# Kernel optimization log

Hardware: AMD Instinct MI355X
Metric: run time of the kernel (lower is better)

## Reference

```python
import jax, jax.numpy as jnp
import numpy as np

N_E = 1024
E_DIM = 256
BETA = 0.25

def setup_inputs() -> dict:
    key = jax.random.key(0)
    k1, k2 = jax.random.split(key)
    z = jax.random.normal(k1, (32, E_DIM, 32, 32), dtype=jnp.float32)
    # embedding initialized uniform(-1/n_e, 1/n_e) as in the torch module
    emb_w = jax.random.uniform(k2, (N_E, E_DIM), dtype=jnp.float32,
                               minval=-1.0 / N_E, maxval=1.0 / N_E)
    return {"z": z, "emb_w": emb_w}

def reference(z, emb_w):
    # z: (B, C, H, W) with C == e_dim
    zp = jnp.transpose(z, (0, 2, 3, 1))          # (B, H, W, C)
    zf = zp.reshape(-1, emb_w.shape[1])           # (N, e_dim)
    # squared L2 distances: ||z||^2 + ||e||^2 - 2 z e^T  -> (N, n_e)
    d = (jnp.sum(zf * zf, axis=1, keepdims=True)
         + jnp.sum(emb_w * emb_w, axis=1)
         - 2.0 * jnp.matmul(zf, emb_w.T))
    idx = jnp.argmin(d, axis=1)                   # (N,)
    min_encoding_indices = idx[:, None]           # (N, 1)
    min_encodings = jax.nn.one_hot(idx, emb_w.shape[0], dtype=zf.dtype)  # (N, n_e)
    z_q = emb_w[idx].reshape(zp.shape)            # gather instead of one-hot matmul
    # VQ loss (stop-gradient on codebook / encoder respectively)
    loss = (jnp.mean((jax.lax.stop_gradient(z_q) - zp) ** 2)
            + BETA * jnp.mean((z_q - jax.lax.stop_gradient(zp)) ** 2))
    # straight-through estimator
    z_q_st = zp + jax.lax.stop_gradient(z_q - zp)
    e_mean = jnp.mean(min_encodings, axis=0)      # (n_e,)
    perplexity = jnp.exp(-jnp.sum(e_mean * jnp.log(e_mean + 1e-10)))
    z_q_out = jnp.transpose(z_q_st, (0, 3, 1, 2)) # (B, C, H, W)
    return (z_q_out, loss, perplexity, min_encodings, min_encoding_indices)
```

## Files before the change

kernel.cpp:

```cpp
#include <hip/hip_runtime.h>
#include <math.h>

#define NROWS 32768
#define NE    1024
#define CDIM  256
#define ZB_STRIDE 262144

#define ZQ_OFF   0
#define LOSS_OFF 8388608
#define PERP_OFF 8388609
#define ENC_OFF  8388610
#define IDX_OFF  41943042

#define THETA 1.0e-4f
#define NEG2_SCALE (-0.00048828125f)

typedef _Float16 f16x8 __attribute__((ext_vector_type(8)));
typedef __attribute__((ext_vector_type(4))) float f32x4;
typedef __attribute__((ext_vector_type(8))) unsigned short ushort8;

__device__ __forceinline__ unsigned short f2h(float x) {
  _Float16 h = (_Float16)x;
  unsigned short u;
  __builtin_memcpy(&u, &h, 2);
  return u;
}

__device__ __forceinline__ float np_sumsq_256_s1(const float* __restrict__ base) {
  float tot[2];
#pragma unroll
  for (int hh = 0; hh < 2; ++hh) {
    float r[8];
#pragma unroll
    for (int j = 0; j < 8; ++j) {
      float x = base[hh * 128 + j];
      r[j] = __fmul_rn(x, x);
    }
    for (int i = 8; i < 128; i += 8) {
#pragma unroll
      for (int j = 0; j < 8; ++j) {
        float x = base[hh * 128 + i + j];
        r[j] = __fadd_rn(r[j], __fmul_rn(x, x));
      }
    }
    tot[hh] = __fadd_rn(__fadd_rn(__fadd_rn(r[0], r[1]), __fadd_rn(r[2], r[3])),
                        __fadd_rn(__fadd_rn(r[4], r[5]), __fadd_rn(r[6], r[7])));
  }
  return __fadd_rn(tot[0], tot[1]);
}

__global__ __launch_bounds__(256) void convert_all(const float* __restrict__ z,
                                                   const float* __restrict__ emb,
                                                   unsigned short* __restrict__ zf16r,
                                                   unsigned short* __restrict__ ef16r,
                                                   float* __restrict__ embT,
                                                   float* __restrict__ znorm,
                                                   float* __restrict__ enorm) {
  __shared__ __align__(16) char smem[38144];
  const int bid = blockIdx.x;
  const int t = threadIdx.x;

  if (bid < 512) {
    unsigned short (*T16)[266] = reinterpret_cast<unsigned short (*)[266]>(smem);
    float (*accsF)[8][16][4] = reinterpret_cast<float (*)[8][16][4]>(smem + 34048);
    const int b = bid >> 4, hwt = bid & 15;
    const int hw0 = hwt * 64;
    const int hw4 = t & 15;
    const int jj = (t >> 4) & 7;
    const int hh = t >> 7;
    const float* zb = z + (size_t)b * ZB_STRIDE + hw0 + hw4 * 4;

    float rr[4];
#pragma unroll
    for (int i = 0; i < 16; ++i) {
      int c = hh * 128 + jj + 8 * i;
      float4 v = *reinterpret_cast<const float4*>(zb + (size_t)c * 1024);
      const float xv[4] = {v.x, v.y, v.z, v.w};
#pragma unroll
      for (int q = 0; q < 4; ++q) {
        float p = __fmul_rn(xv[q], xv[q]);
        rr[q] = (i == 0) ? p : __fadd_rn(rr[q], p);
        T16[hw4 * 4 + q][c] = f2h(xv[q]);
      }
    }
#pragma unroll
    for (int q = 0; q < 4; ++q) accsF[hh][jj][hw4][q] = rr[q];
    __syncthreads();

    if (t < 64) {
      const int h4 = t >> 2, cq = t & 3;
      float tot[2];
#pragma unroll
      for (int half = 0; half < 2; ++half) {
        float r[8];
#pragma unroll
        for (int j = 0; j < 8; ++j) r[j] = accsF[half][j][h4][cq];
        tot[half] = __fadd_rn(__fadd_rn(__fadd_rn(r[0], r[1]), __fadd_rn(r[2], r[3])),
                              __fadd_rn(__fadd_rn(r[4], r[5]), __fadd_rn(r[6], r[7])));
      }
      znorm[b * 1024 + hw0 + t] = __fadd_rn(tot[0], tot[1]);
    }

    const int pw = b * 16 + hwt;
    const int panel = pw >> 1, wrh = pw & 1;
    const int l15w = t & 15, gw = (t >> 4) & 3, miw = t >> 6;
    const int rowW = miw * 16 + l15w;
#pragma unroll
    for (int kc = 0; kc < 8; ++kc) {
      ushort8 o;
#pragma unroll
      for (int el = 0; el < 8; ++el) o[el] = T16[rowW][kc * 32 + gw * 8 + el];
      size_t chunk = ((((size_t)panel * 2 + wrh) * 8 + kc) * 4 + miw) * 64 + (size_t)gw * 16 + l15w;
      *reinterpret_cast<ushort8*>(zf16r + (chunk << 3)) = o;
    }
  } else if (bid < 640) {
    int cid = (bid - 512) * 256 + t;
    int e = cid >> 5, cc = cid & 31;
    int kc = cc >> 2, g = cc & 3;
    int c0 = kc * 32 + g * 8;
    ushort8 o;
#pragma unroll
    for (int el = 0; el < 8; ++el) o[el] = f2h(emb[(size_t)e * 256 + c0 + el] * 4096.0f);
    int et = e >> 7, wcb = (e >> 6) & 1, nj = (e >> 4) & 3, l15e = e & 15;
    size_t chunk = ((((size_t)et * 2 + wcb) * 8 + kc) * 4 + nj) * 64 + (size_t)g * 16 + l15e;
    *reinterpret_cast<ushort8*>(ef16r + (chunk << 3)) = o;
  } else if (bid < 896) {
    float (*tile)[33] = reinterpret_cast<float (*)[33]>(smem);
    int tb = bid - 640;
    int be = tb & 31, bc = tb >> 5;
    int tx = t & 31, ty = t >> 5;
#pragma unroll
    for (int i = 0; i < 4; ++i)
      tile[ty + 8 * i][tx] = emb[(size_t)(be * 32 + ty + 8 * i) * 256 + bc * 32 + tx];
    __syncthreads();
#pragma unroll
    for (int i = 0; i < 4; ++i)
      embT[(size_t)(bc * 32 + ty + 8 * i) * 1024 + be * 32 + tx] = tile[tx][ty + 8 * i];
  } else {
    int n = (bid - 896) * 256 + t;
    enorm[n] = np_sumsq_256_s1(emb + (size_t)n * CDIM);
  }
}

__global__ __launch_bounds__(256, 4) void argmin_tile(
    const unsigned short* __restrict__ zf16r, const unsigned short* __restrict__ ef16r,
    const float* __restrict__ znorm, const float* __restrict__ enorm,
    float* __restrict__ pbd, int* __restrict__ pbi, float* __restrict__ pb2) {
  __shared__ float sdd[128][2];
  __shared__ float sd2[128][2];
  __shared__ int   sdi[128][2];

  const int tid = threadIdx.x;
  const int lane = tid & 63, w = tid >> 6;
  const int wr = w >> 1, wc = w & 1;
  const int l15 = lane & 15, g = lane >> 4;

  const int bid = blockIdx.x;
  const int nb2 = (bid >> 3) & 1;
  const int mb = (bid & 7) * 32 + (bid >> 4);
  const int n0 = mb * 128;

  const unsigned short* bP0 = zf16r + (size_t)(mb * 2 + wc) * 16384 + lane * 8;

  const int n0w = n0 + wc * 64;
  float zn[4];
#pragma unroll
  for (int nj = 0; nj < 4; ++nj) zn[nj] = znorm[n0w + nj * 16 + l15];

  float bd[4], b2[4]; int bi[4];
#pragma unroll
  for (int nj = 0; nj < 4; ++nj) { bd[nj] = 3.4e38f; b2[nj] = 3.4e38f; bi[nj] = 0; }

  const f32x4 z4 = {0.f, 0.f, 0.f, 0.f};
#pragma unroll 1
  for (int et = 0; et < 4; ++et) {
    const unsigned short* aP = ef16r + (size_t)(nb2 * 8 + et * 2 + wr) * 16384 + lane * 8;
    const unsigned short* bP = bP0;

    f32x4 acc[4][4];
#pragma unroll
    for (int ei = 0; ei < 4; ++ei)
#pragma unroll
      for (int nj = 0; nj < 4; ++nj) acc[ei][nj] = z4;

#pragma unroll 1
    for (int kc = 0; kc < 8; ++kc) {
      f16x8 af[4], bv[4];
#pragma unroll
      for (int ei = 0; ei < 4; ++ei)
        af[ei] = *reinterpret_cast<const f16x8*>(aP + ei * 512);
#pragma unroll
      for (int nj = 0; nj < 4; ++nj)
        bv[nj] = *reinterpret_cast<const f16x8*>(bP + nj * 512);
      aP += 2048; bP += 2048;
#pragma unroll
      for (int ei = 0; ei < 4; ++ei)
#pragma unroll
        for (int nj = 0; nj < 4; ++nj)
          acc[ei][nj] = __builtin_amdgcn_mfma_f32_16x16x32_f16(af[ei], bv[nj],
                                                               acc[ei][nj], 0, 0, 0);
    }

    const int e0w = nb2 * 512 + et * 128 + wr * 64;
#pragma unroll
    for (int ei = 0; ei < 4; ++ei)
#pragma unroll
      for (int rg = 0; rg < 4; ++rg) {
        int e = e0w + ei * 16 + g * 4 + rg;
        float en = enorm[e];
#pragma unroll
        for (int nj = 0; nj < 4; ++nj) {
          float d = fmaf(NEG2_SCALE, acc[ei][nj][rg], __fadd_rn(zn[nj], en));
          if (d < bd[nj]) {
            b2[nj] = bd[nj]; bd[nj] = d; bi[nj] = e;
          } else if (d < b2[nj]) {
            b2[nj] = d;
          }
        }
      }
  }

#pragma unroll
  for (int nj = 0; nj < 4; ++nj) {
#pragma unroll
    for (int m = 16; m <= 32; m <<= 1) {
      float od = __shfl_xor(bd[nj], m, 64);
      int   oi = __shfl_xor(bi[nj], m, 64);
      float o2 = __shfl_xor(b2[nj], m, 64);
      float hi = fmaxf(bd[nj], od);
      b2[nj] = fminf(fminf(b2[nj], o2), hi);
      if (od < bd[nj] || (od == bd[nj] && oi < bi[nj])) { bd[nj] = od; bi[nj] = oi; }
    }
    if (g == 0) {
      int nl = wc * 64 + nj * 16 + l15;
      sdd[nl][wr] = bd[nj];
      sdi[nl][wr] = bi[nj];
      sd2[nl][wr] = b2[nj];
    }
  }
  __syncthreads();

  if (tid < 128) {
    float d0 = sdd[tid][0], d1 = sdd[tid][1];
    int   i0 = sdi[tid][0], i1 = sdi[tid][1];
    float s0 = sd2[tid][0], s1 = sd2[tid][1];
    float bdf; int bif;
    if (d1 < d0 || (d1 == d0 && i1 < i0)) { bdf = d1; bif = i1; } else { bdf = d0; bif = i0; }
    float b2f = fminf(fminf(s0, s1), fmaxf(d0, d1));
    size_t o = (size_t)(n0 + tid) * 2 + nb2;
    pbd[o] = bdf; pbi[o] = bif; pb2[o] = b2f;
  }
}

__global__ __launch_bounds__(256) void merge_kernel(
    const float* __restrict__ pbd, const int* __restrict__ pbi,
    const float* __restrict__ pb2,
    int* __restrict__ idx_out, float* __restrict__ loss_blk,
    int* __restrict__ flag_cnt, int* __restrict__ flag_list) {
  __shared__ float red[256];
  const int t = threadIdx.x;
  int n = blockIdx.x * 256 + t;
  float d0 = pbd[(size_t)n * 2], d1 = pbd[(size_t)n * 2 + 1];
  int   i0 = pbi[(size_t)n * 2], i1 = pbi[(size_t)n * 2 + 1];
  float s0 = pb2[(size_t)n * 2], s1 = pb2[(size_t)n * 2 + 1];
  float bd; int bi;
  if (d1 < d0 || (d1 == d0 && i1 < i0)) { bd = d1; bi = i1; } else { bd = d0; bi = i0; }
  float b2 = fminf(fminf(s0, s1), fmaxf(d0, d1));
  idx_out[n] = bi;
  if (b2 - bd < THETA) {
    int p = atomicAdd(flag_cnt, 1);
    flag_list[p] = n;
  }
  red[t] = bd;
  __syncthreads();
  for (int s2 = 128; s2 > 0; s2 >>= 1) {
    if (t < s2) red[t] += red[t + s2];
    __syncthreads();
  }
  if (t == 0) loss_blk[blockIdx.x] = red[0];
}

__global__ __launch_bounds__(256) void repair_kernel(
    const float* __restrict__ z, const float* __restrict__ embT,
    const float* __restrict__ znorm, const float* __restrict__ enorm,
    const int* __restrict__ flag_cnt, const int* __restrict__ flag_list,
    int* __restrict__ idx_out) {
  __shared__ float zrow[4][256];
  __shared__ float rd[256];
  __shared__ int   ri[256];
  const int t = threadIdx.x;
  const int cnt = flag_cnt[0] < NROWS ? flag_cnt[0] : NROWS;
  const int nquad = (cnt + 3) >> 2;
  const float4* embT4 = reinterpret_cast<const float4*>(embT);
  for (int j = blockIdx.x; j < nquad; j += gridDim.x) {
    int nr[4];
    __syncthreads();
#pragma unroll
    for (int r = 0; r < 4; ++r) {
      int jr = j * 4 + r;
      nr[r] = flag_list[jr < cnt ? jr : cnt - 1];
      zrow[r][t] = z[(size_t)(nr[r] >> 10) * ZB_STRIDE + (size_t)t * 1024 + (nr[r] & 1023)];
    }
    __syncthreads();
    float4 dot[4] = {{0.f,0.f,0.f,0.f},{0.f,0.f,0.f,0.f},{0.f,0.f,0.f,0.f},{0.f,0.f,0.f,0.f}};
    for (int k = 0; k < 256; ++k) {
      float4 v = embT4[k * 256 + t];
#pragma unroll
      for (int r = 0; r < 4; ++r) {
        float s = zrow[r][k];
        dot[r].x = fmaf(s, v.x, dot[r].x);
        dot[r].y = fmaf(s, v.y, dot[r].y);
        dot[r].z = fmaf(s, v.z, dot[r].z);
        dot[r].w = fmaf(s, v.w, dot[r].w);
      }
    }
#pragma unroll 1
    for (int r = 0; r < 4; ++r) {
      const float zn = znorm[nr[r]];
      float bd = 3.4e38f; int bi = 0;
      const float dv[4] = {dot[r].x, dot[r].y, dot[r].z, dot[r].w};
#pragma unroll
      for (int q = 0; q < 4; ++q) {
        int e = t * 4 + q;
        float d = __fsub_rn(__fadd_rn(zn, enorm[e]), __fmul_rn(2.0f, dv[q]));
        if (d < bd) { bd = d; bi = e; }
      }
      rd[t] = bd; ri[t] = bi;
      __syncthreads();
      for (int s2 = 128; s2 > 0; s2 >>= 1) {
        if (t < s2) {
          float od = rd[t + s2]; int oi = ri[t + s2];
          if (od < rd[t] || (od == rd[t] && oi < ri[t])) { rd[t] = od; ri[t] = oi; }
        }
        __syncthreads();
      }
      if (t == 0) idx_out[nr[r]] = ri[0];
      __syncthreads();
    }
  }
}

__global__ __launch_bounds__(256) void outputs_kernel(const int* __restrict__ idx,
                                                      const float* __restrict__ emb,
                                                      float* __restrict__ out_enc,
                                                      float* __restrict__ out_idxf,
                                                      int* __restrict__ hist,
                                                      float* __restrict__ zq_out) {
  const int t = threadIdx.x;
  for (int i = blockIdx.x * 256 + t; i < NROWS * 256; i += 2048 * 256) {
    int n = i >> 8, j4 = i & 255;
    int e = idx[n];
    float4 v = {0.f, 0.f, 0.f, 0.f};
    if ((e >> 2) == j4) ((float*)&v)[e & 3] = 1.0f;
    reinterpret_cast<float4*>(out_enc)[i] = v;
  }
  if (blockIdx.x < 1024) {
    __shared__ int   sidx[32];
    __shared__ float erow[32][257];
    int b = blockIdx.x >> 5, h = blockIdx.x & 31;
    if (t < 32) sidx[t] = idx[b * 1024 + h * 32 + t];
    __syncthreads();
    const float4* emb4 = reinterpret_cast<const float4*>(emb);
    int rj = t >> 3, v0 = t & 7;
    int er = sidx[rj];
#pragma unroll
    for (int u = 0; u < 8; ++u) {
      int f4 = v0 + 8 * u;
      float4 vv = emb4[(size_t)er * 64 + f4];
      erow[rj][f4 * 4 + 0] = vv.x;
      erow[rj][f4 * 4 + 1] = vv.y;
      erow[rj][f4 * 4 + 2] = vv.z;
      erow[rj][f4 * 4 + 3] = vv.w;
    }
    __syncthreads();
    int w4 = t & 7, cs = t >> 3;
    float4* zq4 = reinterpret_cast<float4*>(zq_out + (size_t)b * ZB_STRIDE + h * 32);
#pragma unroll
    for (int u = 0; u < 8; ++u) {
      int c = cs + 32 * u;
      float4 o = {erow[w4 * 4 + 0][c], erow[w4 * 4 + 1][c],
                  erow[w4 * 4 + 2][c], erow[w4 * 4 + 3][c]};
      zq4[(size_t)c * 256 + w4] = o;
    }
  } else if (blockIdx.x < 1152) {
    int n = (blockIdx.x - 1024) * 256 + t;
    int e = idx[n];
    out_idxf[n] = (float)e;
    atomicAdd(&hist[e], 1);
  }
}

__global__ __launch_bounds__(256) void finalize_kernel(const float* __restrict__ loss_blk,
                                                       const int* __restrict__ hist,
                                                       float* __restrict__ out_loss,
                                                       float* __restrict__ out_perp) {
  __shared__ float red[256];
  int t = threadIdx.x;
  red[t] = (t < 128) ? loss_blk[t] : 0.f;
  __syncthreads();
  for (int s2 = 128; s2 > 0; s2 >>= 1) {
    if (t < s2) red[t] += red[t + s2];
    __syncthreads();
  }
  if (t == 0) out_loss[0] = 1.25f * (red[0] / 8388608.0f);
  __syncthreads();
  float hs = 0.f;
  for (int i = t; i < 1024; i += 256) {
    float em = (float)hist[i] / 32768.0f;
    hs += em * logf(em + 1e-10f);
  }
  red[t] = hs;
  __syncthreads();
  for (int s2 = 128; s2 > 0; s2 >>= 1) {
    if (t < s2) red[t] += red[t + s2];
    __syncthreads();
  }
  if (t == 0) out_perp[0] = expf(-red[0]);
}

extern "C" void kernel_launch(void* const* d_in, const int* in_sizes, int n_in,
                              void* d_out, int out_size, void* d_ws, size_t ws_size,
                              hipStream_t stream) {
  const float* z   = (const float*)d_in[0];
  const float* emb = (const float*)d_in[1];
  float* out = (float*)d_out;

  float* out_zq   = out + ZQ_OFF;
  float* out_loss = out + LOSS_OFF;
  float* out_perp = out + PERP_OFF;
  float* out_enc  = out + ENC_OFF;
  float* out_idxf = out + IDX_OFF;

  int*   idx       = (int*)d_ws;
  int*   hist      = idx + NROWS;
  int*   flag_cnt  = hist + NE;
  int*   flag_list = flag_cnt + 4;
  float* loss_blk  = (float*)(flag_list + NROWS);
  float* znorm     = loss_blk + 128;
  float* enorm     = znorm + NROWS;

  unsigned short* zf16r = (unsigned short*)(out_enc + 2);
  unsigned short* ef16r = zf16r + (size_t)NROWS * CDIM;
  float*          embT  = (float*)(ef16r + (size_t)NE * CDIM);
  float*          pbd   = embT + 262144;
  int*            pbi   = (int*)(pbd + 65536);
  float*          pb2   = (float*)(pbi + 65536);

  hipMemsetAsync(hist, 0, (NE + 1) * sizeof(int), stream);

  convert_all<<<900, 256, 0, stream>>>(z, emb, zf16r, ef16r, embT, znorm, enorm);
  argmin_tile<<<512, 256, 0, stream>>>(zf16r, ef16r, znorm, enorm, pbd, pbi, pb2);
  merge_kernel<<<NROWS / 256, 256, 0, stream>>>(pbd, pbi, pb2, idx, loss_blk, flag_cnt, flag_list);
  repair_kernel<<<256, 256, 0, stream>>>(z, embT, znorm, enorm, flag_cnt, flag_list, idx);
  outputs_kernel<<<2048, 256, 0, stream>>>(idx, emb, out_enc, out_idxf, hist, out_zq);
  finalize_kernel<<<1, 256, 0, stream>>>(loss_blk, hist, out_loss, out_perp);
}
```

Before: 157.4 us.

## Give each argmin block all codes for 64 rows and drop merge kernel

The argmin kernel now assigns each block 64 rows across all 1024 codes, with the four waves each covering 256 codes, instead of 128 rows across half the codebook. The cross-half merge therefore happens inside the block, and the block writes final indices, flags near-ties and sums loss partials directly. This removes the separate merge kernel launch and the global partial-result buffers. In exchange, each block reuses its z tile over more codes but gets less reuse of the embedding tile, and the loss partials grow to 512 entries, which the finalize kernel now reduces.

```diff
diff --git a/kernel.cpp b/kernel.cpp
--- a/kernel.cpp
+++ b/kernel.cpp
@@ -145,27 +145,25 @@
 __global__ __launch_bounds__(256, 4) void argmin_tile(
     const unsigned short* __restrict__ zf16r, const unsigned short* __restrict__ ef16r,
     const float* __restrict__ znorm, const float* __restrict__ enorm,
-    float* __restrict__ pbd, int* __restrict__ pbi, float* __restrict__ pb2) {
-  __shared__ float sdd[128][2];
-  __shared__ float sd2[128][2];
-  __shared__ int   sdi[128][2];
+    int* __restrict__ idx_out, float* __restrict__ loss_blk,
+    int* __restrict__ flag_cnt, int* __restrict__ flag_list) {
+  __shared__ float sdd[64][4];
+  __shared__ float sd2[64][4];
+  __shared__ int   sdi[64][4];
 
   const int tid = threadIdx.x;
   const int lane = tid & 63, w = tid >> 6;
-  const int wr = w >> 1, wc = w & 1;
   const int l15 = lane & 15, g = lane >> 4;
 
   const int bid = blockIdx.x;
-  const int nb2 = (bid >> 3) & 1;
-  const int mb = (bid & 7) * 32 + (bid >> 4);
-  const int n0 = mb * 128;
-
-  const unsigned short* bP0 = zf16r + (size_t)(mb * 2 + wc) * 16384 + lane * 8;
-
-  const int n0w = n0 + wc * 64;
+  const int mb = (bid & 7) * 64 + (bid >> 3);
+  const int n0 = mb * 64;
+
+  const unsigned short* bP0 = zf16r + (size_t)mb * 16384 + lane * 8;
+
   float zn[4];
 #pragma unroll
-  for (int nj = 0; nj < 4; ++nj) zn[nj] = znorm[n0w + nj * 16 + l15];
+  for (int nj = 0; nj < 4; ++nj) zn[nj] = znorm[n0 + nj * 16 + l15];
 
   float bd[4], b2[4]; int bi[4];
 #pragma unroll
@@ -174,7 +172,7 @@
   const f32x4 z4 = {0.f, 0.f, 0.f, 0.f};
 #pragma unroll 1
   for (int et = 0; et < 4; ++et) {
-    const unsigned short* aP = ef16r + (size_t)(nb2 * 8 + et * 2 + wr) * 16384 + lane * 8;
+    const unsigned short* aP = ef16r + (size_t)(w * 4 + et) * 16384 + lane * 8;
     const unsigned short* bP = bP0;
 
     f32x4 acc[4][4];
@@ -201,7 +199,7 @@
                                                                acc[ei][nj], 0, 0, 0);
     }
 
-    const int e0w = nb2 * 512 + et * 128 + wr * 64;
+    const int e0w = (w * 4 + et) * 64;
 #pragma unroll
     for (int ei = 0; ei < 4; ++ei)
 #pragma unroll
@@ -232,52 +230,39 @@
       if (od < bd[nj] || (od == bd[nj] && oi < bi[nj])) { bd[nj] = od; bi[nj] = oi; }
     }
     if (g == 0) {
-      int nl = wc * 64 + nj * 16 + l15;
-      sdd[nl][wr] = bd[nj];
-      sdi[nl][wr] = bi[nj];
-      sd2[nl][wr] = b2[nj];
+      int nl = nj * 16 + l15;
+      sdd[nl][w] = bd[nj];
+      sdi[nl][w] = bi[nj];
+      sd2[nl][w] = b2[nj];
     }
   }
   __syncthreads();
 
-  if (tid < 128) {
-    float d0 = sdd[tid][0], d1 = sdd[tid][1];
-    int   i0 = sdi[tid][0], i1 = sdi[tid][1];
-    float s0 = sd2[tid][0], s1 = sd2[tid][1];
-    float bdf; int bif;
-    if (d1 < d0 || (d1 == d0 && i1 < i0)) { bdf = d1; bif = i1; } else { bdf = d0; bif = i0; }
-    float b2f = fminf(fminf(s0, s1), fmaxf(d0, d1));
-    size_t o = (size_t)(n0 + tid) * 2 + nb2;
-    pbd[o] = bdf; pbi[o] = bif; pb2[o] = b2f;
-  }
-}
-
-__global__ __launch_bounds__(256) void merge_kernel(
-    const float* __restrict__ pbd, const int* __restrict__ pbi,
-    const float* __restrict__ pb2,
-    int* __restrict__ idx_out, float* __restrict__ loss_blk,
-    int* __restrict__ flag_cnt, int* __restrict__ flag_list) {
-  __shared__ float red[256];
-  const int t = threadIdx.x;
-  int n = blockIdx.x * 256 + t;
-  float d0 = pbd[(size_t)n * 2], d1 = pbd[(size_t)n * 2 + 1];
-  int   i0 = pbi[(size_t)n * 2], i1 = pbi[(size_t)n * 2 + 1];
-  float s0 = pb2[(size_t)n * 2], s1 = pb2[(size_t)n * 2 + 1];
-  float bd; int bi;
-  if (d1 < d0 || (d1 == d0 && i1 < i0)) { bd = d1; bi = i1; } else { bd = d0; bi = i0; }
-  float b2 = fminf(fminf(s0, s1), fmaxf(d0, d1));
-  idx_out[n] = bi;
-  if (b2 - bd < THETA) {
-    int p = atomicAdd(flag_cnt, 1);
-    flag_list[p] = n;
-  }
-  red[t] = bd;
-  __syncthreads();
-  for (int s2 = 128; s2 > 0; s2 >>= 1) {
-    if (t < s2) red[t] += red[t + s2];
-    __syncthreads();
-  }
-  if (t == 0) loss_blk[blockIdx.x] = red[0];
+  if (tid < 64) {
+    float bdf = 3.4e38f; int bif = 0x7FFFFFFF; int bw = -1;
+#pragma unroll
+    for (int ww = 0; ww < 4; ++ww) {
+      float d = sdd[tid][ww];
+      int   i = sdi[tid][ww];
+      if (d < bdf || (d == bdf && i < bif)) { bdf = d; bif = i; bw = ww; }
+    }
+    float b2f = 3.4e38f;
+#pragma unroll
+    for (int ww = 0; ww < 4; ++ww) {
+      float v = (ww == bw) ? sd2[tid][ww] : sdd[tid][ww];
+      b2f = fminf(b2f, v);
+    }
+    int n = n0 + tid;
+    idx_out[n] = bif;
+    if (b2f - bdf < THETA) {
+      int p = atomicAdd(flag_cnt, 1);
+      flag_list[p] = n;
+    }
+    float s = bdf;
+#pragma unroll
+    for (int m = 1; m <= 32; m <<= 1) s += __shfl_xor(s, m, 64);
+    if (tid == 0) loss_blk[bid] = s;
+  }
 }
 
 __global__ __launch_bounds__(256) void repair_kernel(
@@ -396,7 +381,7 @@
                                                        float* __restrict__ out_perp) {
   __shared__ float red[256];
   int t = threadIdx.x;
-  red[t] = (t < 128) ? loss_blk[t] : 0.f;
+  red[t] = loss_blk[t] + loss_blk[t + 256];
   __syncthreads();
   for (int s2 = 128; s2 > 0; s2 >>= 1) {
     if (t < s2) red[t] += red[t + s2];
@@ -436,21 +421,18 @@
   int*   flag_cnt  = hist + NE;
   int*   flag_list = flag_cnt + 4;
   float* loss_blk  = (float*)(flag_list + NROWS);
-  float* znorm     = loss_blk + 128;
+  float* znorm     = loss_blk + 512;
   float* enorm     = znorm + NROWS;
 
   unsigned short* zf16r = (unsigned short*)(out_enc + 2);
   unsigned short* ef16r = zf16r + (size_t)NROWS * CDIM;
   float*          embT  = (float*)(ef16r + (size_t)NE * CDIM);
-  float*          pbd   = embT + 262144;
-  int*            pbi   = (int*)(pbd + 65536);
-  float*          pb2   = (float*)(pbi + 65536);
 
   hipMemsetAsync(hist, 0, (NE + 1) * sizeof(int), stream);
 
   convert_all<<<900, 256, 0, stream>>>(z, emb, zf16r, ef16r, embT, znorm, enorm);
-  argmin_tile<<<512, 256, 0, stream>>>(zf16r, ef16r, znorm, enorm, pbd, pbi, pb2);
-  merge_kernel<<<NROWS / 256, 256, 0, stream>>>(pbd, pbi, pb2, idx, loss_blk, flag_cnt, flag_list);
+  argmin_tile<<<512, 256, 0, stream>>>(zf16r, ef16r, znorm, enorm,
+                                       idx, loss_blk, flag_cnt, flag_list);
   repair_kernel<<<256, 256, 0, stream>>>(z, embT, znorm, enorm, flag_cnt, flag_list, idx);
   outputs_kernel<<<2048, 256, 0, stream>>>(idx, emb, out_enc, out_idxf, hist, out_zq);
   finalize_kernel<<<1, 256, 0, stream>>>(loss_blk, hist, out_loss, out_perp);
```

Result: faster. 153.4 us (-2.6%).
